# Kernel tuning notes

Hardware: AMD Instinct MI355X
Metric: run time of the kernel (lower is better)

The kernel has to match this reference:

```python
import jax, jax.numpy as jnp
import numpy as np

B, V, C, K, E = 4, 50000, 128, 128, 400000
H = 128  # mlp hidden width


def setup_inputs() -> dict:
    key = jax.random.key(0)
    ks = jax.random.split(key, 16)
    return {
        "x_in": jax.random.normal(ks[0], (B, V, C), jnp.float32),
        "mass": jax.random.uniform(ks[1], (B, V), jnp.float32) + 0.1,
        "L": jnp.zeros((1,), jnp.float32),  # unused by spectral diffusion
        "evals": jax.random.uniform(ks[2], (B, K), jnp.float32),
        "evecs": jax.random.normal(ks[3], (B, V, K), jnp.float32) / np.sqrt(V),
        "grad_rows": jax.random.randint(ks[4], (B, E), 0, V, jnp.int32),
        "grad_cols": jax.random.randint(ks[5], (B, E), 0, V, jnp.int32),
        "gradX_vals": jax.random.normal(ks[6], (B, E), jnp.float32),
        "gradY_vals": jax.random.normal(ks[7], (B, E), jnp.float32),
        # learned parameters
        "diffusion_time": jax.random.uniform(ks[8], (C,), jnp.float32) * 0.1 + 1e-3,
        "A_re": jax.random.normal(ks[9], (C, C), jnp.float32) / np.sqrt(C),
        "A_im": jax.random.normal(ks[10], (C, C), jnp.float32) / np.sqrt(C),
        "W0": jax.random.normal(ks[11], (3 * C, H), jnp.float32) / np.sqrt(3 * C),
        "b0": jnp.zeros((H,), jnp.float32),
        "W1": jax.random.normal(ks[12], (H, C), jnp.float32) / np.sqrt(H),
        "b1": jnp.zeros((C,), jnp.float32),
    }


def _spmm(rows, cols, vals, x):
    # sparse [V,V] (COO) @ x [V,C] via gather + segment_sum
    return jax.ops.segment_sum(vals[:, None] * x[cols], rows, num_segments=x.shape[0])


def reference(x_in, mass, L, evals, evecs, grad_rows, grad_cols,
              gradX_vals, gradY_vals, diffusion_time, A_re, A_im,
              W0, b0, W1, b1):
    # LearnedTimeDiffusion (spectral): project, decay, unproject
    t = jnp.clip(diffusion_time, 1e-8)  # torch clamps min=1e-8
    x_spec = jnp.einsum('bvk,bvc->bkc', evecs, mass[..., None] * x_in)
    x_spec = x_spec * jnp.exp(-evals[:, :, None] * t[None, None, :])
    x_diffuse = jnp.einsum('bvk,bkc->bvc', evecs, x_spec)  # [B,V,C]

    # per-sample sparse gradient operators (batched via vmap)
    gx = jax.vmap(_spmm)(grad_rows, grad_cols, gradX_vals, x_diffuse)  # [B,V,C]
    gy = jax.vmap(_spmm)(grad_rows, grad_cols, gradY_vals, x_diffuse)  # [B,V,C]

    # SpatialGradientFeatures with gradient rotations (complex inner product)
    vB_re = gx @ A_re - gy @ A_im
    vB_im = gy @ A_re + gx @ A_im
    x_grad_features = jnp.tanh(gx * vB_re + gy * vB_im)

    # MiniMLP (dropout off / eval mode) + residual
    feat = jnp.concatenate([x_in, x_diffuse, x_grad_features], axis=-1)  # [B,V,3C]
    h = jax.nn.relu(feat @ W0 + b0)
    return h @ W1 + b1 + x_in
```

## Files before the change

### kernel.cpp

```cpp
#include <hip/hip_runtime.h>

#define BB 4
#define VV 50000
#define CC 128
#define KK 128
#define EE 400000
#define HH 128

#define CHUNK 512
#define NCHUNK 98
#define PROJ_NCH 64
#define TILES_PER_B 1563
#define NT64 782

typedef unsigned short u16;
typedef short bf16x8 __attribute__((ext_vector_type(8)));
typedef float f32x4 __attribute__((ext_vector_type(4)));

__device__ __forceinline__ u16 f2bf(float f) {
    union { float f; unsigned u; } x; x.f = f;
    unsigned r = x.u + 0x7FFFu + ((x.u >> 16) & 1u);
    return (u16)(r >> 16);
}
__device__ __forceinline__ float bf2f(u16 u) {
    union { unsigned u; float f; } x; x.u = ((unsigned)u) << 16;
    return x.f;
}
__device__ __forceinline__ unsigned pack2(float lo, float hi) {
    return ((unsigned)f2bf(hi) << 16) | (unsigned)f2bf(lo);
}
__device__ __forceinline__ float tanh_fast(float u) {
    float uc = fminf(fmaxf(u, -15.f), 15.f);
    float e = __expf(-2.f * uc);
    return (1.f - e) / (1.f + e);
}
__device__ __forceinline__ f32x4 fma4(float s, float4 v, f32x4 a) {
    a.x = fmaf(s, v.x, a.x);
    a.y = fmaf(s, v.y, a.y);
    a.z = fmaf(s, v.z, a.z);
    a.w = fmaf(s, v.w, a.w);
    return a;
}

__global__ void k_zero_u32(unsigned int* __restrict__ p, int n) {
    int i = blockIdx.x * blockDim.x + threadIdx.x;
    if (i < n) p[i] = 0u;
}

__global__ void k_hist(const int* __restrict__ rows, int* __restrict__ hist) {
    int idx = blockIdx.x * blockDim.x + threadIdx.x;
    if (idx >= BB * EE) return;
    int b = idx / EE;
    atomicAdd(&hist[b * VV + rows[idx]], 1);
}

__global__ __launch_bounds__(512) void k_scan1(const int* __restrict__ hist,
                                               int* __restrict__ rs,
                                               int* __restrict__ csum) {
    __shared__ int sh[512];
    int bc = blockIdx.x;
    int b = bc / NCHUNK, ch = bc % NCHUNK;
    int base = ch * CHUNK;
    int t = threadIdx.x;
    int v = base + t;
    int h = (v < VV) ? hist[b * VV + v] : 0;
    sh[t] = h;
    __syncthreads();
#pragma unroll
    for (int off = 1; off < 512; off <<= 1) {
        int val = (t >= off) ? sh[t - off] : 0;
        __syncthreads();
        if (t >= off) sh[t] += val;
        __syncthreads();
    }
    int incl = sh[t];
    if (v < VV) rs[b * VV + v] = incl - h;
    if (t == 511) csum[b * 128 + ch] = incl;
}

__global__ __launch_bounds__(512) void k_scan2(int* __restrict__ csum) {
    __shared__ int sh[BB][NCHUNK];
    int t = threadIdx.x;
    int b = t / NCHUNK, ch = t % NCHUNK;
    if (t < BB * NCHUNK) sh[b][ch] = csum[b * 128 + ch];
    __syncthreads();
    if (t < BB) {
        int run = 0;
#pragma unroll 2
        for (int c = 0; c < NCHUNK; ++c) {
            int v = sh[t][c];
            sh[t][c] = run;
            run += v;
        }
    }
    __syncthreads();
    if (t < BB * NCHUNK) csum[b * 128 + ch] = sh[b][ch];
}

__global__ void k_scan3(int* __restrict__ rs, const int* __restrict__ csum,
                        int* __restrict__ cursor) {
    int idx = blockIdx.x * blockDim.x + threadIdx.x;
    if (idx >= BB * VV) return;
    int b = idx / VV, v = idx % VV;
    int r = rs[idx] + csum[b * 128 + v / CHUNK];
    rs[idx] = r;
    cursor[idx] = r;
}

__global__ void k_bucket(const int* __restrict__ rows, int* __restrict__ cursor,
                         int* __restrict__ edge_idx) {
    int idx = blockIdx.x * blockDim.x + threadIdx.x;
    if (idx >= BB * EE) return;
    int b = idx / EE, e = idx % EE;
    int r = rows[idx];
    int p = atomicAdd(&cursor[b * VV + r], 1);
    edge_idx[(size_t)b * EE + p] = e;
}

__global__ void k_pack_rot(const float* __restrict__ Are, const float* __restrict__ Aim,
                           u16* __restrict__ Wre_p, u16* __restrict__ Wim_p) {
    int f = blockIdx.x * blockDim.x + threadIdx.x;
    if (f >= 4096) return;
    int lane = f & 63;
    int s = (f >> 6) & 7;
    int t = f >> 9;
    int n = t * 16 + (lane & 15);
#pragma unroll
    for (int j = 0; j < 8; ++j) {
        int k = s * 32 + ((lane >> 4) << 3) + j;
        float re, im;
        if (k < 128) { re = Are[k * CC + n];           im = Aim[k * CC + n]; }
        else         { re = -Aim[(k - 128) * CC + n];  im = Are[(k - 128) * CC + n]; }
        Wre_p[(size_t)f * 8 + j] = f2bf(re);
        Wim_p[(size_t)f * 8 + j] = f2bf(im);
    }
}

__global__ void k_pack_w0(const float* __restrict__ W0, u16* __restrict__ W0p) {
    int f = blockIdx.x * blockDim.x + threadIdx.x;
    if (f >= 6144) return;
    int lane = f & 63;
    int rem = f % 768;
    int s = rem >> 6;
    int t = f / 768;
    int n = t * 16 + (lane & 15);
#pragma unroll
    for (int j = 0; j < 8; ++j) {
        int k = s * 32 + ((lane >> 4) << 3) + j;
        W0p[(size_t)f * 8 + j] = f2bf(W0[(size_t)k * HH + n]);
    }
}

__global__ void k_pack_w1(const float* __restrict__ W1, u16* __restrict__ W1p) {
    int f = blockIdx.x * blockDim.x + threadIdx.x;
    if (f >= 2048) return;
    int lane = f & 63;
    int s = (f >> 6) & 3;
    int t = f >> 8;
    int n = t * 16 + (lane & 15);
#pragma unroll
    for (int j = 0; j < 8; ++j) {
        int k = s * 32 + ((lane >> 4) << 3) + j;
        W1p[(size_t)f * 8 + j] = f2bf(W1[(size_t)k * CC + n]);
    }
}

__global__ __launch_bounds__(512) void k_project(
        const float* __restrict__ x_in, const float* __restrict__ mass,
        const float* __restrict__ evecs, float* __restrict__ spec) {
    __shared__ float evs[16][128];
    __shared__ float xs[16][128];
    int b  = blockIdx.x >> 6;
    int ch = blockIdx.x & 63;
    const int rowsPer = (VV + PROJ_NCH - 1) / PROJ_NCH;
    int vbase = ch * rowsPer;
    int vend  = min(vbase + rowsPer, VV);
    int t = threadIdx.x;
    int tk = t >> 5, tc = t & 31;
    int lrow = tk;
    int lc4  = tc * 4;

    f32x4 a0 = {0,0,0,0}, a1 = {0,0,0,0}, a2 = {0,0,0,0}, a3 = {0,0,0,0};
    f32x4 a4 = {0,0,0,0}, a5 = {0,0,0,0}, a6 = {0,0,0,0}, a7 = {0,0,0,0};

    float4 xr = make_float4(0.f, 0.f, 0.f, 0.f);
    float4 er = make_float4(0.f, 0.f, 0.f, 0.f);
    float  mr = 0.f;
    {
        int v = vbase + lrow;
        if (v < vend) {
            xr = *(const float4*)&x_in[((size_t)b * VV + v) * CC + lc4];
            er = *(const float4*)&evecs[((size_t)b * VV + v) * KK + lc4];
            mr = mass[b * VV + v];
        }
    }

    for (int v0 = vbase; v0 < vend; v0 += 16) {
        __syncthreads();
        *(float4*)&xs[lrow][lc4]  = make_float4(xr.x * mr, xr.y * mr, xr.z * mr, xr.w * mr);
        *(float4*)&evs[lrow][lc4] = er;
        __syncthreads();
        if (v0 + 16 < vend) {
            int v = v0 + 16 + lrow;
            if (v < vend) {
                xr = *(const float4*)&x_in[((size_t)b * VV + v) * CC + lc4];
                er = *(const float4*)&evecs[((size_t)b * VV + v) * KK + lc4];
                mr = mass[b * VV + v];
            } else {
                xr = make_float4(0.f, 0.f, 0.f, 0.f);
                er = make_float4(0.f, 0.f, 0.f, 0.f);
                mr = 0.f;
            }
        }
#pragma unroll
        for (int vv = 0; vv < 16; ++vv) {
            float4 xv = *(const float4*)&xs[vv][tc * 4];
            float4 ea = *(const float4*)&evs[vv][tk * 8];
            float4 eb = *(const float4*)&evs[vv][tk * 8 + 4];
            a0 = fma4(ea.x, xv, a0);
            a1 = fma4(ea.y, xv, a1);
            a2 = fma4(ea.z, xv, a2);
            a3 = fma4(ea.w, xv, a3);
            a4 = fma4(eb.x, xv, a4);
            a5 = fma4(eb.y, xv, a5);
            a6 = fma4(eb.z, xv, a6);
            a7 = fma4(eb.w, xv, a7);
        }
    }

    {
        size_t base = ((size_t)b * KK + tk * 8) * CC + tc * 4;
        float* p0 = &spec[base];
        atomicAdd(p0 + 0, a0.x); atomicAdd(p0 + 1, a0.y); atomicAdd(p0 + 2, a0.z); atomicAdd(p0 + 3, a0.w);
        float* p1 = p0 + CC;
        atomicAdd(p1 + 0, a1.x); atomicAdd(p1 + 1, a1.y); atomicAdd(p1 + 2, a1.z); atomicAdd(p1 + 3, a1.w);
        float* p2 = p0 + 2 * CC;
        atomicAdd(p2 + 0, a2.x); atomicAdd(p2 + 1, a2.y); atomicAdd(p2 + 2, a2.z); atomicAdd(p2 + 3, a2.w);
        float* p3 = p0 + 3 * CC;
        atomicAdd(p3 + 0, a3.x); atomicAdd(p3 + 1, a3.y); atomicAdd(p3 + 2, a3.z); atomicAdd(p3 + 3, a3.w);
        float* p4 = p0 + 4 * CC;
        atomicAdd(p4 + 0, a4.x); atomicAdd(p4 + 1, a4.y); atomicAdd(p4 + 2, a4.z); atomicAdd(p4 + 3, a4.w);
        float* p5 = p0 + 5 * CC;
        atomicAdd(p5 + 0, a5.x); atomicAdd(p5 + 1, a5.y); atomicAdd(p5 + 2, a5.z); atomicAdd(p5 + 3, a5.w);
        float* p6 = p0 + 6 * CC;
        atomicAdd(p6 + 0, a6.x); atomicAdd(p6 + 1, a6.y); atomicAdd(p6 + 2, a6.z); atomicAdd(p6 + 3, a6.w);
        float* p7 = p0 + 7 * CC;
        atomicAdd(p7 + 0, a7.x); atomicAdd(p7 + 1, a7.y); atomicAdd(p7 + 2, a7.z); atomicAdd(p7 + 3, a7.w);
    }
}

__global__ void k_decay(const float* __restrict__ spec, const float* __restrict__ evals,
                        const float* __restrict__ dt, float* __restrict__ spec_d) {
    int idx = blockIdx.x * blockDim.x + threadIdx.x;
    if (idx >= BB * KK * CC) return;
    int c = idx & 127;
    int k = (idx >> 7) & 127;
    int b = idx >> 14;
    float t = fmaxf(dt[c], 1e-8f);
    spec_d[idx] = spec[idx] * expf(-evals[b * KK + k] * t);
}

__global__ __launch_bounds__(256) void k_unproject(
        const float* __restrict__ evecs, const float* __restrict__ spec_d,
        u16* __restrict__ xd) {
    __shared__ float ss[128][128];
    __shared__ float evs[32][128];
    int b = blockIdx.x / TILES_PER_B;
    int vbase = (blockIdx.x % TILES_PER_B) * 32;
    int t = threadIdx.x;

#pragma unroll
    for (int l = 0; l < 16; ++l) {
        int idx4 = l * 256 + t;
        int row = idx4 >> 5;
        int c4 = (idx4 & 31) * 4;
        *(float4*)&ss[row][c4] = *(const float4*)&spec_d[((size_t)b * KK + row) * CC + c4];
    }
#pragma unroll
    for (int l = 0; l < 4; ++l) {
        int idx4 = l * 256 + t;
        int row = idx4 >> 5;
        int c4 = (idx4 & 31) * 4;
        int v = vbase + row;
        float4 e4 = make_float4(0.f, 0.f, 0.f, 0.f);
        if (v < VV) e4 = *(const float4*)&evecs[((size_t)b * VV + v) * KK + c4];
        *(float4*)&evs[row][c4] = e4;
    }
    __syncthreads();

    int cg = t & 31, vg = t >> 5;
    int c4 = cg * 4;
    float acc[4][4];
#pragma unroll
    for (int i = 0; i < 4; ++i)
#pragma unroll
        for (int q = 0; q < 4; ++q) acc[i][q] = 0.f;

#pragma unroll 8
    for (int k = 0; k < 128; ++k) {
        float4 s = *(float4*)&ss[k][c4];
#pragma unroll
        for (int i = 0; i < 4; ++i) {
            float ev = evs[vg * 4 + i][k];
            acc[i][0] = fmaf(ev, s.x, acc[i][0]);
            acc[i][1] = fmaf(ev, s.y, acc[i][1]);
            acc[i][2] = fmaf(ev, s.z, acc[i][2]);
            acc[i][3] = fmaf(ev, s.w, acc[i][3]);
        }
    }
#pragma unroll
    for (int i = 0; i < 4; ++i) {
        int v = vbase + vg * 4 + i;
        if (v < VV) {
            uint2 o;
            o.x = pack2(acc[i][0], acc[i][1]);
            o.y = pack2(acc[i][2], acc[i][3]);
            *(uint2*)&xd[(((size_t)b * VV + v) << 7) + c4] = o;
        }
    }
}

__global__ __launch_bounds__(256) void k_rowgather(
        const int* __restrict__ cols, const float* __restrict__ vxv,
        const float* __restrict__ vyv, const int* __restrict__ edge_idx,
        const int* __restrict__ rs, const int* __restrict__ cursor,
        const u16* __restrict__ xd, u16* __restrict__ gx, u16* __restrict__ gy) {
    int w = blockIdx.x * 4 + (threadIdx.x >> 6);
    int lane = threadIdx.x & 63;
    int b = w / VV;
    int beg = rs[w], end = cursor[w];
    float ax0 = 0.f, ax1 = 0.f, ay0 = 0.f, ay1 = 0.f;
    size_t ebase = (size_t)b * EE;
    const int* eb = edge_idx + ebase;
    const int* cb = cols + ebase;
    const float* fxb = vxv + ebase;
    const float* fyb = vyv + ebase;
    const u16* xdb = xd + (((size_t)b * VV) << 7) + lane * 2;
    int i = beg;
    for (; i + 4 <= end; i += 4) {
        int e0 = eb[i], e1 = eb[i + 1], e2 = eb[i + 2], e3 = eb[i + 3];
        int c0 = cb[e0], c1 = cb[e1], c2 = cb[e2], c3 = cb[e3];
        float fx0 = fxb[e0], fx1 = fxb[e1], fx2 = fxb[e2], fx3 = fxb[e3];
        float fy0 = fyb[e0], fy1 = fyb[e1], fy2 = fyb[e2], fy3 = fyb[e3];
        unsigned u0 = *(const unsigned*)&xdb[(size_t)c0 << 7];
        unsigned u1 = *(const unsigned*)&xdb[(size_t)c1 << 7];
        unsigned u2 = *(const unsigned*)&xdb[(size_t)c2 << 7];
        unsigned u3 = *(const unsigned*)&xdb[(size_t)c3 << 7];
        float x0, x1;
        x0 = bf2f((u16)(u0 & 0xFFFFu)); x1 = bf2f((u16)(u0 >> 16));
        ax0 = fmaf(fx0, x0, ax0); ax1 = fmaf(fx0, x1, ax1);
        ay0 = fmaf(fy0, x0, ay0); ay1 = fmaf(fy0, x1, ay1);
        x0 = bf2f((u16)(u1 & 0xFFFFu)); x1 = bf2f((u16)(u1 >> 16));
        ax0 = fmaf(fx1, x0, ax0); ax1 = fmaf(fx1, x1, ax1);
        ay0 = fmaf(fy1, x0, ay0); ay1 = fmaf(fy1, x1, ay1);
        x0 = bf2f((u16)(u2 & 0xFFFFu)); x1 = bf2f((u16)(u2 >> 16));
        ax0 = fmaf(fx2, x0, ax0); ax1 = fmaf(fx2, x1, ax1);
        ay0 = fmaf(fy2, x0, ay0); ay1 = fmaf(fy2, x1, ay1);
        x0 = bf2f((u16)(u3 & 0xFFFFu)); x1 = bf2f((u16)(u3 >> 16));
        ax0 = fmaf(fx3, x0, ax0); ax1 = fmaf(fx3, x1, ax1);
        ay0 = fmaf(fy3, x0, ay0); ay1 = fmaf(fy3, x1, ay1);
    }
    for (; i < end; ++i) {
        int e0 = eb[i];
        int c0 = cb[e0];
        float fx0 = fxb[e0], fy0 = fyb[e0];
        unsigned u0 = *(const unsigned*)&xdb[(size_t)c0 << 7];
        float x0 = bf2f((u16)(u0 & 0xFFFFu)), x1 = bf2f((u16)(u0 >> 16));
        ax0 = fmaf(fx0, x0, ax0); ax1 = fmaf(fx0, x1, ax1);
        ay0 = fmaf(fy0, x0, ay0); ay1 = fmaf(fy0, x1, ay1);
    }
    size_t ro = ((size_t)w << 7) + lane * 2;
    *(unsigned*)&gx[ro] = pack2(ax0, ax1);
    *(unsigned*)&gy[ro] = pack2(ay0, ay1);
}

__global__ __launch_bounds__(256) void k_gradfeat(
        const u16* __restrict__ gx, const u16* __restrict__ gy,
        const u16* __restrict__ Wre_p, const u16* __restrict__ Wim_p,
        u16* __restrict__ xgf) {
    __shared__ u16 Gs[64][264];
    __shared__ u16 Bre[8][64][8];
    __shared__ u16 Bim[8][64][8];
    int b = blockIdx.x / NT64;
    int vbase = (blockIdx.x % NT64) * 64;
    int t = threadIdx.x;
    int lane = t & 63, w = t >> 6;
    {
        int row = t >> 2, p = t & 3;
        int v = vbase + row;
        bool ok = v < VV;
        size_t ro = ((size_t)b * VV + (ok ? v : 0)) << 7;
        const uint4* gxr = (const uint4*)&gx[ro + p * 32];
        const uint4* gyr = (const uint4*)&gy[ro + p * 32];
        uint4 z = make_uint4(0u, 0u, 0u, 0u);
#pragma unroll
        for (int i = 0; i < 4; ++i) {
            uint4 a = ok ? gxr[i] : z;
            uint4 c = ok ? gyr[i] : z;
            *(uint4*)&Gs[row][p * 32 + i * 8] = a;
            *(uint4*)&Gs[row][128 + p * 32 + i * 8] = c;
        }
    }
    __syncthreads();
    int m = lane & 15, q = lane >> 4;
    bf16x8 afr[8];
#pragma unroll
    for (int s = 0; s < 8; ++s)
        afr[s] = *(const bf16x8*)&Gs[w * 16 + m][s * 32 + q * 8];

    for (int tt = 0; tt < 8; ++tt) {
        __syncthreads();
        {
            const uint4* sre = (const uint4*)&Wre_p[(size_t)tt * 4096];
            const uint4* sim = (const uint4*)&Wim_p[(size_t)tt * 4096];
            uint4* dre = (uint4*)&Bre[0][0][0];
            uint4* dim = (uint4*)&Bim[0][0][0];
            dre[t] = sre[t]; dre[t + 256] = sre[t + 256];
            dim[t] = sim[t]; dim[t + 256] = sim[t + 256];
        }
        __syncthreads();
        f32x4 are = {0.f, 0.f, 0.f, 0.f};
        f32x4 aim = {0.f, 0.f, 0.f, 0.f};
#pragma unroll
        for (int s = 0; s < 8; ++s) {
            bf16x8 br = *(const bf16x8*)&Bre[s][lane][0];
            bf16x8 bi = *(const bf16x8*)&Bim[s][lane][0];
            are = __builtin_amdgcn_mfma_f32_16x16x32_bf16(afr[s], br, are, 0, 0, 0);
            aim = __builtin_amdgcn_mfma_f32_16x16x32_bf16(afr[s], bi, aim, 0, 0, 0);
        }
#pragma unroll
        for (int r = 0; r < 4; ++r) {
            int row = w * 16 + q * 4 + r;
            int v = vbase + row;
            if (v < VV) {
                float gxv = bf2f(Gs[row][tt * 16 + m]);
                float gyv = bf2f(Gs[row][128 + tt * 16 + m]);
                float u = gxv * are[r] + gyv * aim[r];
                xgf[(((size_t)b * VV + v) << 7) + tt * 16 + m] = f2bf(tanh_fast(u));
            }
        }
    }
}

__global__ __launch_bounds__(256) void k_mlp(
        const float* __restrict__ x_in, const u16* __restrict__ xd,
        const u16* __restrict__ xgf,
        const u16* __restrict__ W0p, const float* __restrict__ b0,
        const u16* __restrict__ W1p, const float* __restrict__ b1,
        float* __restrict__ out) {
    __shared__ u16 Fs[64][392];
    __shared__ u16 Hs[64][136];
    __shared__ u16 Bs[12][64][8];
    int b = blockIdx.x / NT64;
    int vbase = (blockIdx.x % NT64) * 64;
    int t = threadIdx.x;
    int lane = t & 63, w = t >> 6;
    {
        int row = t >> 2, p = t & 3;
        int v = vbase + row;
        bool ok = v < VV;
        size_t ro = ((size_t)b * VV + (ok ? v : 0)) << 7;
        const float4* xir = (const float4*)&x_in[ro + p * 32];
#pragma unroll
        for (int i = 0; i < 8; ++i) {
            float4 f = ok ? xir[i] : make_float4(0.f, 0.f, 0.f, 0.f);
            uint2 u;
            u.x = pack2(f.x, f.y);
            u.y = pack2(f.z, f.w);
            *(uint2*)&Fs[row][p * 32 + i * 4] = u;
        }
        const uint4* xdr = (const uint4*)&xd[ro + p * 32];
        const uint4* xgr = (const uint4*)&xgf[ro + p * 32];
        uint4 z = make_uint4(0u, 0u, 0u, 0u);
#pragma unroll
        for (int i = 0; i < 4; ++i) {
            uint4 a = ok ? xdr[i] : z;
            uint4 c = ok ? xgr[i] : z;
            *(uint4*)&Fs[row][128 + p * 32 + i * 8] = a;
            *(uint4*)&Fs[row][256 + p * 32 + i * 8] = c;
        }
    }
    __syncthreads();
    int m = lane & 15, q = lane >> 4;
    bf16x8 af[12];
#pragma unroll
    for (int s = 0; s < 12; ++s)
        af[s] = *(const bf16x8*)&Fs[w * 16 + m][s * 32 + q * 8];

    for (int tt = 0; tt < 8; ++tt) {
        __syncthreads();
        {
            const uint4* src = (const uint4*)&W0p[(size_t)tt * 6144];
            uint4* d = (uint4*)&Bs[0][0][0];
            d[t] = src[t];
            d[t + 256] = src[t + 256];
            d[t + 512] = src[t + 512];
        }
        __syncthreads();
        f32x4 acc = {0.f, 0.f, 0.f, 0.f};
#pragma unroll
        for (int s = 0; s < 12; ++s) {
            bf16x8 bb = *(const bf16x8*)&Bs[s][lane][0];
            acc = __builtin_amdgcn_mfma_f32_16x16x32_bf16(af[s], bb, acc, 0, 0, 0);
        }
        float bias = b0[tt * 16 + m];
#pragma unroll
        for (int r = 0; r < 4; ++r) {
            Hs[w * 16 + q * 4 + r][tt * 16 + m] = f2bf(fmaxf(acc[r] + bias, 0.f));
        }
    }

    bf16x8 ah[4];
    for (int tt = 0; tt < 8; ++tt) {
        __syncthreads();
        {
            const uint4* src = (const uint4*)&W1p[(size_t)tt * 2048];
            uint4* d = (uint4*)&Bs[0][0][0];
            d[t] = src[t];
        }
        if (tt == 0) {
#pragma unroll
            for (int s = 0; s < 4; ++s)
                ah[s] = *(const bf16x8*)&Hs[w * 16 + m][s * 32 + q * 8];
        }
        __syncthreads();
        f32x4 acc = {0.f, 0.f, 0.f, 0.f};
#pragma unroll
        for (int s = 0; s < 4; ++s) {
            bf16x8 bb = *(const bf16x8*)&Bs[s][lane][0];
            acc = __builtin_amdgcn_mfma_f32_16x16x32_bf16(ah[s], bb, acc, 0, 0, 0);
        }
        float bias = b1[tt * 16 + m];
#pragma unroll
        for (int r = 0; r < 4; ++r) {
            int row = w * 16 + q * 4 + r;
            int v = vbase + row;
            if (v < VV) {
                size_t off = (((size_t)b * VV + v) << 7) + tt * 16 + m;
                out[off] = acc[r] + bias + x_in[off];
            }
        }
    }
}

extern "C" void kernel_launch(void* const* d_in, const int* in_sizes, int n_in,
                              void* d_out, int out_size, void* d_ws, size_t ws_size,
                              hipStream_t stream) {
    (void)in_sizes; (void)n_in; (void)out_size; (void)ws_size;
    const float* x_in  = (const float*)d_in[0];
    const float* mass  = (const float*)d_in[1];
    const float* evals = (const float*)d_in[3];
    const float* evecs = (const float*)d_in[4];
    const int* grad_rows = (const int*)d_in[5];
    const int* grad_cols = (const int*)d_in[6];
    const float* gX = (const float*)d_in[7];
    const float* gY = (const float*)d_in[8];
    const float* dt  = (const float*)d_in[9];
    const float* Are = (const float*)d_in[10];
    const float* Aim = (const float*)d_in[11];
    const float* W0 = (const float*)d_in[12];
    const float* b0 = (const float*)d_in[13];
    const float* W1 = (const float*)d_in[14];
    const float* b1 = (const float*)d_in[15];
    float* out = (float*)d_out;

    char* w = (char*)d_ws;
    u16* xd  = (u16*)w; w += (size_t)BB * VV * CC * 2;
    u16* gx  = (u16*)w; w += (size_t)BB * VV * CC * 2;
    u16* gy  = (u16*)w; w += (size_t)BB * VV * CC * 2;
    u16* xgf = (u16*)w; w += (size_t)BB * VV * CC * 2;
    float* spec   = (float*)w; w += (size_t)BB * KK * CC * 4;
    float* spec_d = (float*)w; w += (size_t)BB * KK * CC * 4;
    int* hist   = (int*)w; w += (size_t)BB * VV * 4;
    int* rs     = (int*)w; w += (size_t)BB * VV * 4;
    int* cursor = (int*)w; w += (size_t)BB * VV * 4;
    int* csum   = (int*)w; w += (size_t)BB * 128 * 4;
    int* edge_idx = (int*)w; w += (size_t)BB * EE * 4;
    u16* Wre_p = (u16*)w; w += (size_t)4096 * 8 * 2;
    u16* Wim_p = (u16*)w; w += (size_t)4096 * 8 * 2;
    u16* W0p   = (u16*)w; w += (size_t)6144 * 8 * 2;
    u16* W1p   = (u16*)w; w += (size_t)2048 * 8 * 2;

    hipLaunchKernelGGL(k_zero_u32, dim3((BB * VV + 255) / 256), dim3(256), 0, stream,
                       (unsigned int*)hist, BB * VV);
    hipLaunchKernelGGL(k_zero_u32, dim3((BB * KK * CC + 255) / 256), dim3(256), 0, stream,
                       (unsigned int*)spec, BB * KK * CC);
    hipLaunchKernelGGL(k_hist, dim3((BB * EE + 255) / 256), dim3(256), 0, stream,
                       grad_rows, hist);
    hipLaunchKernelGGL(k_scan1, dim3(BB * NCHUNK), dim3(512), 0, stream, hist, rs, csum);
    hipLaunchKernelGGL(k_scan2, dim3(1), dim3(512), 0, stream, csum);
    hipLaunchKernelGGL(k_scan3, dim3((BB * VV + 255) / 256), dim3(256), 0, stream,
                       rs, csum, cursor);
    hipLaunchKernelGGL(k_bucket, dim3((BB * EE + 255) / 256), dim3(256), 0, stream,
                       grad_rows, cursor, edge_idx);
    hipLaunchKernelGGL(k_pack_rot, dim3(16), dim3(256), 0, stream, Are, Aim, Wre_p, Wim_p);
    hipLaunchKernelGGL(k_pack_w0, dim3(24), dim3(256), 0, stream, W0, W0p);
    hipLaunchKernelGGL(k_pack_w1, dim3(8), dim3(256), 0, stream, W1, W1p);
    hipLaunchKernelGGL(k_project, dim3(BB * PROJ_NCH), dim3(512), 0, stream,
                       x_in, mass, evecs, spec);
    hipLaunchKernelGGL(k_decay, dim3((BB * KK * CC + 255) / 256), dim3(256), 0, stream,
                       spec, evals, dt, spec_d);
    hipLaunchKernelGGL(k_unproject, dim3(BB * TILES_PER_B), dim3(256), 0, stream,
                       evecs, spec_d, xd);
    hipLaunchKernelGGL(k_rowgather, dim3(BB * VV / 4), dim3(256), 0, stream,
                       grad_cols, gX, gY, edge_idx, rs, cursor, xd, gx, gy);
    hipLaunchKernelGGL(k_gradfeat, dim3(BB * NT64), dim3(256), 0, stream,
                       gx, gy, Wre_p, Wim_p, xgf);
    hipLaunchKernelGGL(k_mlp, dim3(BB * NT64), dim3(256), 0, stream,
                       x_in, xd, xgf, W0p, b0, W1p, b1, out);
}
```

Before: 1.014 ms.

## Load MLP operands directly from global into MFMA registers, drop LDS staging

The MLP kernel no longer stages the 64x384 feature tile or the weight slices in shared memory. Each wave loads its own A fragments straight from global memory, converting x_in to bf16 in registers, and reads the pre-packed weight fragments directly from global (L2-cached). The hidden tile becomes per-wave, so all block-level __syncthreads are removed. This cuts LDS traffic, shared memory footprint and barriers, which should raise occupancy. The cost is less coalesced, redundant per-wave global reads of the weights.

Result: no change. 1.027 ms (+1.3%).

```diff
diff --git a/kernel.cpp b/kernel.cpp
--- a/kernel.cpp
+++ b/kernel.cpp
@@ -40,6 +40,14 @@
     a.z = fmaf(s, v.z, a.z);
     a.w = fmaf(s, v.w, a.w);
     return a;
+}
+__device__ __forceinline__ bf16x8 cvt8(float4 a, float4 b) {
+    union { unsigned u[4]; bf16x8 v; } r;
+    r.u[0] = pack2(a.x, a.y);
+    r.u[1] = pack2(a.z, a.w);
+    r.u[2] = pack2(b.x, b.y);
+    r.u[3] = pack2(b.z, b.w);
+    return r.v;
 }
 
 __global__ void k_zero_u32(unsigned int* __restrict__ p, int n) {
@@ -448,86 +456,60 @@
         const u16* __restrict__ W0p, const float* __restrict__ b0,
         const u16* __restrict__ W1p, const float* __restrict__ b1,
         float* __restrict__ out) {
-    __shared__ u16 Fs[64][392];
-    __shared__ u16 Hs[64][136];
-    __shared__ u16 Bs[12][64][8];
+    __shared__ u16 Hs[4][16][136];
     int b = blockIdx.x / NT64;
     int vbase = (blockIdx.x % NT64) * 64;
     int t = threadIdx.x;
     int lane = t & 63, w = t >> 6;
-    {
-        int row = t >> 2, p = t & 3;
-        int v = vbase + row;
-        bool ok = v < VV;
-        size_t ro = ((size_t)b * VV + (ok ? v : 0)) << 7;
-        const float4* xir = (const float4*)&x_in[ro + p * 32];
-#pragma unroll
-        for (int i = 0; i < 8; ++i) {
-            float4 f = ok ? xir[i] : make_float4(0.f, 0.f, 0.f, 0.f);
-            uint2 u;
-            u.x = pack2(f.x, f.y);
-            u.y = pack2(f.z, f.w);
-            *(uint2*)&Fs[row][p * 32 + i * 4] = u;
-        }
-        const uint4* xdr = (const uint4*)&xd[ro + p * 32];
-        const uint4* xgr = (const uint4*)&xgf[ro + p * 32];
-        uint4 z = make_uint4(0u, 0u, 0u, 0u);
-#pragma unroll
-        for (int i = 0; i < 4; ++i) {
-            uint4 a = ok ? xdr[i] : z;
-            uint4 c = ok ? xgr[i] : z;
-            *(uint4*)&Fs[row][128 + p * 32 + i * 8] = a;
-            *(uint4*)&Fs[row][256 + p * 32 + i * 8] = c;
-        }
-    }
-    __syncthreads();
     int m = lane & 15, q = lane >> 4;
+
+    int rowA = w * 16 + m;
+    int vA = vbase + rowA;
+    int vAc = (vA < VV) ? vA : (VV - 1);
+    size_t roA = ((size_t)b * VV + vAc) << 7;
+
     bf16x8 af[12];
 #pragma unroll
-    for (int s = 0; s < 12; ++s)
-        af[s] = *(const bf16x8*)&Fs[w * 16 + m][s * 32 + q * 8];
-
+    for (int s = 0; s < 4; ++s) {
+        float4 f0 = *(const float4*)&x_in[roA + s * 32 + q * 8];
+        float4 f1 = *(const float4*)&x_in[roA + s * 32 + q * 8 + 4];
+        af[s] = cvt8(f0, f1);
+    }
+#pragma unroll
+    for (int s = 0; s < 4; ++s)
+        af[4 + s] = *(const bf16x8*)&xd[roA + s * 32 + q * 8];
+#pragma unroll
+    for (int s = 0; s < 4; ++s)
+        af[8 + s] = *(const bf16x8*)&xgf[roA + s * 32 + q * 8];
+
+    const u16* w0l = W0p + (size_t)lane * 8;
     for (int tt = 0; tt < 8; ++tt) {
-        __syncthreads();
-        {
-            const uint4* src = (const uint4*)&W0p[(size_t)tt * 6144];
-            uint4* d = (uint4*)&Bs[0][0][0];
-            d[t] = src[t];
-            d[t + 256] = src[t + 256];
-            d[t + 512] = src[t + 512];
-        }
-        __syncthreads();
         f32x4 acc = {0.f, 0.f, 0.f, 0.f};
+        const u16* wp = w0l + (size_t)tt * 6144;
 #pragma unroll
         for (int s = 0; s < 12; ++s) {
-            bf16x8 bb = *(const bf16x8*)&Bs[s][lane][0];
+            bf16x8 bb = *(const bf16x8*)&wp[s * 512];
             acc = __builtin_amdgcn_mfma_f32_16x16x32_bf16(af[s], bb, acc, 0, 0, 0);
         }
         float bias = b0[tt * 16 + m];
 #pragma unroll
         for (int r = 0; r < 4; ++r) {
-            Hs[w * 16 + q * 4 + r][tt * 16 + m] = f2bf(fmaxf(acc[r] + bias, 0.f));
+            Hs[w][q * 4 + r][tt * 16 + m] = f2bf(fmaxf(acc[r] + bias, 0.f));
         }
     }
 
     bf16x8 ah[4];
+#pragma unroll
+    for (int s = 0; s < 4; ++s)
+        ah[s] = *(const bf16x8*)&Hs[w][m][s * 32 + q * 8];
+
+    const u16* w1l = W1p + (size_t)lane * 8;
     for (int tt = 0; tt < 8; ++tt) {
-        __syncthreads();
-        {
-            const uint4* src = (const uint4*)&W1p[(size_t)tt * 2048];
-            uint4* d = (uint4*)&Bs[0][0][0];
-            d[t] = src[t];
-        }
-        if (tt == 0) {
-#pragma unroll
-            for (int s = 0; s < 4; ++s)
-                ah[s] = *(const bf16x8*)&Hs[w * 16 + m][s * 32 + q * 8];
-        }
-        __syncthreads();
         f32x4 acc = {0.f, 0.f, 0.f, 0.f};
+        const u16* wp = w1l + (size_t)tt * 2048;
 #pragma unroll
         for (int s = 0; s < 4; ++s) {
-            bf16x8 bb = *(const bf16x8*)&Bs[s][lane][0];
+            bf16x8 bb = *(const bf16x8*)&wp[s * 512];
             acc = __builtin_amdgcn_mfma_f32_16x16x32_bf16(ah[s], bb, acc, 0, 0, 0);
         }
         float bias = b1[tt * 16 + m];
```
